# Performance work log

Measured on AMD Instinct MI355X. Metric: run time of the kernel, lower is better.

The kernel has to match this reference:

```python
import jax, jax.numpy as jnp
import numpy as np

N, D, E = 50000, 128, 800000
EPS = 1e-5


def setup_inputs() -> dict:
    key = jax.random.key(0)
    ks = jax.random.split(key, 16)
    x = jax.random.normal(ks[0], (N, D), dtype=jnp.float32)
    edge_index = jax.random.randint(ks[1], (2, E), 0, N, dtype=jnp.int32)
    s = 1.0 / np.sqrt(D)
    inp = {"x": x, "edge_index": edge_index}
    for i in range(3):
        inp[f"lng{i}"] = jnp.ones((D,), jnp.float32)
        inp[f"lnb{i}"] = jnp.zeros((D,), jnp.float32)
        inp[f"W{i}"] = jax.random.normal(ks[2 + 2 * i], (D, D), jnp.float32) * s
        inp[f"b{i}"] = jnp.zeros((D,), jnp.float32)
    return inp


def _gcn_norm(edge_index):
    # PyG GCNConv default: add self loops, symmetric normalization D^-1/2 (A+I) D^-1/2
    loop = jnp.arange(N, dtype=edge_index.dtype)
    src = jnp.concatenate([edge_index[0], loop])  # [E+N]
    dst = jnp.concatenate([edge_index[1], loop])
    deg = jax.ops.segment_sum(jnp.ones_like(dst, jnp.float32), dst, num_segments=N)
    dinv = jnp.where(deg > 0, jax.lax.rsqrt(jnp.maximum(deg, 1.0)), 0.0)
    norm = dinv[src] * dinv[dst]  # [E+N]
    return src, dst, norm


def _layer(h, g, bt, W, b, src, dst, norm):
    # LayerNorm -> ReLU -> GCNConv
    mu = jnp.mean(h, axis=-1, keepdims=True)
    var = jnp.mean(jnp.square(h - mu), axis=-1, keepdims=True)
    hn = (h - mu) * jax.lax.rsqrt(var + EPS) * g + bt
    hn = jax.nn.relu(hn) @ W  # [N, D]
    msg = norm[:, None] * hn[src]  # [E+N, D] gather
    return jax.ops.segment_sum(msg, dst, num_segments=N) + b


def reference(x, edge_index, lng0, lnb0, W0, b0, lng1, lnb1, W1, b1, lng2, lnb2, W2, b2):
    src, dst, norm = _gcn_norm(edge_index)
    # conv0 (GCNLayer) + residual
    x = _layer(x, lng0, lnb0, W0, b0, src, dst, norm) + x
    # conv1 (ResGCNLayer: two GCNLayers) + residual
    h = _layer(x, lng1, lnb1, W1, b1, src, dst, norm)
    h = _layer(h, lng2, lnb2, W2, b2, src, dst, norm)
    return h + x
```

## Files before the change

### kernel.cpp

```cpp
#include <hip/hip_runtime.h>

#define N_NODES 50000
#define DIM     128
#define E_EDGES 800000
#define ELLW    64

typedef __attribute__((ext_vector_type(8))) short short8;
typedef __attribute__((ext_vector_type(4))) float f32x4;

__device__ __forceinline__ float bflo(unsigned int u){ return __uint_as_float(u << 16); }
__device__ __forceinline__ float bfhi(unsigned int u){ return __uint_as_float(u & 0xFFFF0000u); }
__device__ __forceinline__ unsigned int f2bf(float f){
  unsigned int u = __float_as_uint(f);
  return (u + 0x7FFFu + ((u >> 16) & 1u)) >> 16;
}
__device__ __forceinline__ unsigned int pack2(float a, float b){
  return f2bf(a) | (f2bf(b) << 16);
}


__global__ __launch_bounds__(256) void count_kernel(const int* __restrict__ edges,
                                                    int* __restrict__ cnt){
  int e = blockIdx.x * 256 + threadIdx.x;
  if (e < E_EDGES) atomicAdd(&cnt[edges[E_EDGES + e]], 1);
}

__global__ __launch_bounds__(256) void dinv_pad_kernel(const int* __restrict__ cnt,
                                                       float* __restrict__ dinv,
                                                       int2* __restrict__ ell){
  int i = blockIdx.x * 256 + threadIdx.x;
  if (i >= N_NODES) return;
  int deg = cnt[i];
  dinv[i] = rsqrtf((float)(deg + 1));
  int2 pad; pad.x = i; pad.y = 0;
  size_t base = (size_t)i * ELLW + deg;
  ell[base + 0] = pad;
  ell[base + 1] = pad;
  ell[base + 2] = pad;
  ell[base + 3] = pad;
}

__global__ __launch_bounds__(256) void fill_kernel(const int* __restrict__ edges,
                                                   int* __restrict__ cur,
                                                   const float* __restrict__ dinv,
                                                   int2* __restrict__ ell){
  int e = blockIdx.x * 256 + threadIdx.x;
  if (e < E_EDGES){
    int s = edges[e];
    int d = edges[E_EDGES + e];
    int pos = atomicAdd(&cur[d], 1);
    int2 pk; pk.x = s; pk.y = __float_as_int(dinv[s] * dinv[d]);
    ell[(size_t)d * ELLW + pos] = pk;
  }
}

__global__ __launch_bounds__(256) void cvtw_all(const float* __restrict__ W0,
                                                const float* __restrict__ W1,
                                                const float* __restrict__ W2,
                                                unsigned short* __restrict__ Wt){
  int idx = blockIdx.x * 256 + threadIdx.x;
  int w = idx >> 14, r = idx & 16383;
  const float* W = (w == 0) ? W0 : (w == 1) ? W1 : W2;
  int k = r >> 7, n = r & 127;
  Wt[w * 16384 + n * 128 + k] = (unsigned short)f2bf(W[r]);
}


__global__ __launch_bounds__(256) void gemm_ln_mfma(const float* __restrict__ X,
                                                    const float* __restrict__ g,
                                                    const float* __restrict__ bt,
                                                    const unsigned short* __restrict__ Wt,
                                                    unsigned short* __restrict__ Y){
  __shared__ unsigned short ldsb[128 * 136];
  int tid = threadIdx.x;
  #pragma unroll
  for (int it = 0; it < 8; ++it){
    int c  = tid + it * 256;
    int n  = c >> 4, kc = c & 15;
    *(short8*)&ldsb[n * 136 + kc * 8] = *(const short8*)(Wt + n * 128 + kc * 8);
  }
  int wave = tid >> 6, lane = tid & 63, quad = lane >> 4, l15 = lane & 15;
  int rowbase = blockIdx.x * 128 + wave * 32;
  int rm0 = rowbase + l15;      if (rm0 > N_NODES - 1) rm0 = N_NODES - 1;
  int rm1 = rowbase + 16 + l15; if (rm1 > N_NODES - 1) rm1 = N_NODES - 1;

  float v0[4][8], v1[4][8];
  float s0 = 0.f, ss0 = 0.f, s1 = 0.f, ss1 = 0.f;
  #pragma unroll
  for (int kk = 0; kk < 4; ++kk){
    float4 xa = *(const float4*)(X + (size_t)rm0 * 128 + kk * 32 + quad * 8);
    float4 xb = *(const float4*)(X + (size_t)rm0 * 128 + kk * 32 + quad * 8 + 4);
    float4 ya = *(const float4*)(X + (size_t)rm1 * 128 + kk * 32 + quad * 8);
    float4 yb_ = *(const float4*)(X + (size_t)rm1 * 128 + kk * 32 + quad * 8 + 4);
    v0[kk][0]=xa.x; v0[kk][1]=xa.y; v0[kk][2]=xa.z; v0[kk][3]=xa.w;
    v0[kk][4]=xb.x; v0[kk][5]=xb.y; v0[kk][6]=xb.z; v0[kk][7]=xb.w;
    v1[kk][0]=ya.x; v1[kk][1]=ya.y; v1[kk][2]=ya.z; v1[kk][3]=ya.w;
    v1[kk][4]=yb_.x; v1[kk][5]=yb_.y; v1[kk][6]=yb_.z; v1[kk][7]=yb_.w;
    #pragma unroll
    for (int j = 0; j < 8; ++j){
      s0 += v0[kk][j]; ss0 += v0[kk][j] * v0[kk][j];
      s1 += v1[kk][j]; ss1 += v1[kk][j] * v1[kk][j];
    }
  }
  s0 += __shfl_xor(s0, 16, 64); ss0 += __shfl_xor(ss0, 16, 64);
  s0 += __shfl_xor(s0, 32, 64); ss0 += __shfl_xor(ss0, 32, 64);
  s1 += __shfl_xor(s1, 16, 64); ss1 += __shfl_xor(ss1, 16, 64);
  s1 += __shfl_xor(s1, 32, 64); ss1 += __shfl_xor(ss1, 32, 64);
  float mu0 = s0 * (1.0f/128.0f), var0 = ss0 * (1.0f/128.0f) - mu0*mu0;
  float mu1 = s1 * (1.0f/128.0f), var1 = ss1 * (1.0f/128.0f) - mu1*mu1;
  float rs0 = rsqrtf(var0 + 1e-5f), rs1 = rsqrtf(var1 + 1e-5f);

  short8 a0[4], a1[4];
  #pragma unroll
  for (int kk = 0; kk < 4; ++kk){
    float4 ga = *(const float4*)(g  + kk * 32 + quad * 8);
    float4 gb = *(const float4*)(g  + kk * 32 + quad * 8 + 4);
    float4 ba = *(const float4*)(bt + kk * 32 + quad * 8);
    float4 bb = *(const float4*)(bt + kk * 32 + quad * 8 + 4);
    float gg[8] = {ga.x,ga.y,ga.z,ga.w,gb.x,gb.y,gb.z,gb.w};
    float bbv[8] = {ba.x,ba.y,ba.z,ba.w,bb.x,bb.y,bb.z,bb.w};
    #pragma unroll
    for (int j = 0; j < 8; ++j){
      float h0 = fmaxf((v0[kk][j] - mu0) * rs0 * gg[j] + bbv[j], 0.0f);
      float h1 = fmaxf((v1[kk][j] - mu1) * rs1 * gg[j] + bbv[j], 0.0f);
      a0[kk][j] = (short)f2bf(h0);
      a1[kk][j] = (short)f2bf(h1);
    }
  }

  f32x4 acc[2][8];
  #pragma unroll
  for (int mt = 0; mt < 2; ++mt)
    #pragma unroll
    for (int nt = 0; nt < 8; ++nt) acc[mt][nt] = (f32x4){0.f, 0.f, 0.f, 0.f};
  __syncthreads();
  #pragma unroll
  for (int kk = 0; kk < 4; ++kk){
    #pragma unroll
    for (int nt = 0; nt < 8; ++nt){
      short8 b = *(const short8*)&ldsb[(nt * 16 + l15) * 136 + kk * 32 + quad * 8];
      acc[0][nt] = __builtin_amdgcn_mfma_f32_16x16x32_bf16(a0[kk], b, acc[0][nt], 0, 0, 0);
      acc[1][nt] = __builtin_amdgcn_mfma_f32_16x16x32_bf16(a1[kk], b, acc[1][nt], 0, 0, 0);
    }
  }
  #pragma unroll
  for (int mt = 0; mt < 2; ++mt)
    #pragma unroll
    for (int nt = 0; nt < 8; ++nt)
      #pragma unroll
      for (int r = 0; r < 4; ++r){
        int row = rowbase + mt * 16 + quad * 4 + r;
        if (row < N_NODES)
          Y[(size_t)row * 128 + nt * 16 + l15] = (unsigned short)f2bf(acc[mt][nt][r]);
      }
}


__global__ __launch_bounds__(256) void gemm_mfma(const unsigned short* __restrict__ A,
                                                 const unsigned short* __restrict__ Wt,
                                                 unsigned short* __restrict__ Y){
  __shared__ unsigned short ldsb[128 * 136];
  int tid = threadIdx.x;
  #pragma unroll
  for (int it = 0; it < 8; ++it){
    int c  = tid + it * 256;
    int n  = c >> 4, kc = c & 15;
    *(short8*)&ldsb[n * 136 + kc * 8] = *(const short8*)(Wt + n * 128 + kc * 8);
  }
  int wave = tid >> 6, lane = tid & 63, quad = lane >> 4, l15 = lane & 15;
  int rowbase = blockIdx.x * 128 + wave * 32;
  int rm0 = rowbase + l15;      if (rm0 > N_NODES - 1) rm0 = N_NODES - 1;
  int rm1 = rowbase + 16 + l15; if (rm1 > N_NODES - 1) rm1 = N_NODES - 1;

  short8 a0[4], a1[4];
  #pragma unroll
  for (int kk = 0; kk < 4; ++kk){
    a0[kk] = *(const short8*)(A + (size_t)rm0 * 128 + kk * 32 + quad * 8);
    a1[kk] = *(const short8*)(A + (size_t)rm1 * 128 + kk * 32 + quad * 8);
  }
  f32x4 acc[2][8];
  #pragma unroll
  for (int mt = 0; mt < 2; ++mt)
    #pragma unroll
    for (int nt = 0; nt < 8; ++nt) acc[mt][nt] = (f32x4){0.f, 0.f, 0.f, 0.f};
  __syncthreads();
  #pragma unroll
  for (int kk = 0; kk < 4; ++kk){
    #pragma unroll
    for (int nt = 0; nt < 8; ++nt){
      short8 b = *(const short8*)&ldsb[(nt * 16 + l15) * 136 + kk * 32 + quad * 8];
      acc[0][nt] = __builtin_amdgcn_mfma_f32_16x16x32_bf16(a0[kk], b, acc[0][nt], 0, 0, 0);
      acc[1][nt] = __builtin_amdgcn_mfma_f32_16x16x32_bf16(a1[kk], b, acc[1][nt], 0, 0, 0);
    }
  }
  #pragma unroll
  for (int mt = 0; mt < 2; ++mt)
    #pragma unroll
    for (int nt = 0; nt < 8; ++nt)
      #pragma unroll
      for (int r = 0; r < 4; ++r){
        int row = rowbase + mt * 16 + quad * 4 + r;
        if (row < N_NODES)
          Y[(size_t)row * 128 + nt * 16 + l15] = (unsigned short)f2bf(acc[mt][nt][r]);
      }
}


template<bool HAS_RES, bool DO_LN>
__global__ __launch_bounds__(256) void agg_kernel(const unsigned short* __restrict__ y,
                                                  const int* __restrict__ cnt,
                                                  const int2* __restrict__ ell,
                                                  const float* __restrict__ dinv,
                                                  const float* __restrict__ bias,
                                                  const float* __restrict__ res,
                                                  float* __restrict__ outp,
                                                  const float* __restrict__ lng,
                                                  const float* __restrict__ lnb,
                                                  unsigned short* __restrict__ hn_out){
  int wid  = (blockIdx.x * 256 + threadIdx.x) >> 6;
  int lane = threadIdx.x & 63;
  if (wid >= N_NODES) return;
  const unsigned int* y32 = (const unsigned int*)y;

  float di = dinv[wid];
  float ws = di * di;
  unsigned int us = y32[(size_t)wid * 64 + lane];
  float a0 = ws * bflo(us);
  float a1 = ws * bfhi(us);

  int deg = cnt[wid];
  int nb  = (deg + 3) >> 2;
  const int2* row = ell + (size_t)wid * ELLW;

  if (nb > 0){
    int2 c0[4]; unsigned int g0[4];
    #pragma unroll
    for (int j = 0; j < 4; ++j) c0[j] = row[j];
    #pragma unroll
    for (int j = 0; j < 4; ++j) g0[j] = y32[(size_t)c0[j].x * 64 + lane];
    for (int b = 1; b < nb; ++b){
      int2 c1[4]; unsigned int g1[4];
      #pragma unroll
      for (int j = 0; j < 4; ++j) c1[j] = row[b * 4 + j];
      #pragma unroll
      for (int j = 0; j < 4; ++j) g1[j] = y32[(size_t)c1[j].x * 64 + lane];
      #pragma unroll
      for (int j = 0; j < 4; ++j){
        float w = __int_as_float(c0[j].y);
        a0 += w * bflo(g0[j]); a1 += w * bfhi(g0[j]);
      }
      #pragma unroll
      for (int j = 0; j < 4; ++j){ c0[j] = c1[j]; g0[j] = g1[j]; }
    }
    #pragma unroll
    for (int j = 0; j < 4; ++j){
      float w = __int_as_float(c0[j].y);
      a0 += w * bflo(g0[j]); a1 += w * bfhi(g0[j]);
    }
  }

  float2 ub2 = ((const float2*)bias)[lane];
  a0 += ub2.x; a1 += ub2.y;
  if (HAS_RES){
    float2 ur = ((const float2*)res)[(size_t)wid * 64 + lane];
    a0 += ur.x; a1 += ur.y;
  }
  if (outp){
    float2 o; o.x = a0; o.y = a1;
    ((float2*)outp)[(size_t)wid * 64 + lane] = o;
  }

  if (DO_LN){
    float s = a0 + a1, ss = a0 * a0 + a1 * a1;
    #pragma unroll
    for (int d = 32; d >= 1; d >>= 1){ s += __shfl_xor(s, d, 64); ss += __shfl_xor(ss, d, 64); }
    float mu  = s * (1.0f / 128.0f);
    float var = ss * (1.0f / 128.0f) - mu * mu;
    float rs  = rsqrtf(var + 1e-5f);
    float2 ug = ((const float2*)lng)[lane];
    float2 ubb = ((const float2*)lnb)[lane];
    float h0 = fmaxf((a0 - mu) * rs * ug.x + ubb.x, 0.0f);
    float h1 = fmaxf((a1 - mu) * rs * ug.y + ubb.y, 0.0f);
    ((unsigned int*)hn_out)[(size_t)wid * 64 + lane] = pack2(h0, h1);
  }
}


extern "C" void kernel_launch(void* const* d_in, const int* in_sizes, int n_in,
                              void* d_out, int out_size, void* d_ws, size_t ws_size,
                              hipStream_t stream){
  const float* x    = (const float*)d_in[0];
  const int*   edges= (const int*)d_in[1];
  const float* lng0 = (const float*)d_in[2];
  const float* lnb0 = (const float*)d_in[3];
  const float* W0   = (const float*)d_in[4];
  const float* b0   = (const float*)d_in[5];
  const float* lng1 = (const float*)d_in[6];
  const float* lnb1 = (const float*)d_in[7];
  const float* W1   = (const float*)d_in[8];
  const float* b1   = (const float*)d_in[9];
  const float* lng2 = (const float*)d_in[10];
  const float* lnb2 = (const float*)d_in[11];
  const float* W2   = (const float*)d_in[12];
  const float* b2   = (const float*)d_in[13];

  char* p = (char*)d_ws;
  auto carve = [&](size_t bytes) -> void* {
    void* r = (void*)p;
    p += (bytes + 255) & ~(size_t)255;
    return r;
  };
  int*   cnt   = (int*)  carve(2 * N_NODES * 4);
  int*   cur   = cnt + N_NODES;
  float* dinv  = (float*)carve(N_NODES * 4);
  int2*  ell   = (int2*) carve((size_t)N_NODES * ELLW * 8);
  unsigned short* Wt = (unsigned short*)carve(3 * 128 * 128 * 2);
  unsigned short* hn = (unsigned short*)carve((size_t)N_NODES * 128 * 2);
  unsigned short* yb = (unsigned short*)carve((size_t)N_NODES * 128 * 2);
  float* out = (float*)d_out;

  hipMemsetAsync(cnt, 0, 2 * N_NODES * 4, stream);

  count_kernel<<<(E_EDGES + 255) / 256, 256, 0, stream>>>(edges, cnt);
  dinv_pad_kernel<<<(N_NODES + 255) / 256, 256, 0, stream>>>(cnt, dinv, ell);
  fill_kernel<<<(E_EDGES + 255) / 256, 256, 0, stream>>>(edges, cur, dinv, ell);
  cvtw_all<<<192, 256, 0, stream>>>(W0, W1, W2, Wt);

  const int GEMM_GRID = (N_NODES + 127) / 128;
  const int ROW_GRID  = (N_NODES + 3) / 4;

  gemm_ln_mfma<<<GEMM_GRID, 256, 0, stream>>>(x, lng0, lnb0, Wt, yb);
  agg_kernel<true, true><<<ROW_GRID, 256, 0, stream>>>(yb, cnt, ell, dinv,
                                                       b0, x, out, lng1, lnb1, hn);
  gemm_mfma<<<GEMM_GRID, 256, 0, stream>>>(hn, Wt + 16384, yb);
  agg_kernel<false, true><<<ROW_GRID, 256, 0, stream>>>(yb, cnt, ell, dinv,
                                                        b1, nullptr, nullptr, lng2, lnb2, hn);
  gemm_mfma<<<GEMM_GRID, 256, 0, stream>>>(hn, Wt + 32768, yb);
  agg_kernel<true, false><<<ROW_GRID, 256, 0, stream>>>(yb, cnt, ell, dinv,
                                                        b2, out, out, nullptr, nullptr, nullptr);
}
```

Measured before the change: 335.3 us.

## Aggregate two nodes per wavefront with wider gathers and memset-zeroed ELL padding

```diff
diff --git a/kernel.cpp b/kernel.cpp
--- a/kernel.cpp
+++ b/kernel.cpp
@@ -25,19 +25,10 @@
   if (e < E_EDGES) atomicAdd(&cnt[edges[E_EDGES + e]], 1);
 }
 
-__global__ __launch_bounds__(256) void dinv_pad_kernel(const int* __restrict__ cnt,
-                                                       float* __restrict__ dinv,
-                                                       int2* __restrict__ ell){
+__global__ __launch_bounds__(256) void dinv_kernel(const int* __restrict__ cnt,
+                                                   float* __restrict__ dinv){
   int i = blockIdx.x * 256 + threadIdx.x;
-  if (i >= N_NODES) return;
-  int deg = cnt[i];
-  dinv[i] = rsqrtf((float)(deg + 1));
-  int2 pad; pad.x = i; pad.y = 0;
-  size_t base = (size_t)i * ELLW + deg;
-  ell[base + 0] = pad;
-  ell[base + 1] = pad;
-  ell[base + 2] = pad;
-  ell[base + 3] = pad;
+  if (i < N_NODES) dinv[i] = rsqrtf((float)(cnt[i] + 1));
 }
 
 __global__ __launch_bounds__(256) void fill_kernel(const int* __restrict__ edges,
@@ -217,71 +208,78 @@
                                                   const float* __restrict__ lng,
                                                   const float* __restrict__ lnb,
                                                   unsigned short* __restrict__ hn_out){
-  int wid  = (blockIdx.x * 256 + threadIdx.x) >> 6;
+  int pair = (blockIdx.x * 256 + threadIdx.x) >> 6;
   int lane = threadIdx.x & 63;
-  if (wid >= N_NODES) return;
-  const unsigned int* y32 = (const unsigned int*)y;
-
-  float di = dinv[wid];
+  int half = lane >> 5, hl = lane & 31;
+  int node = pair * 2 + half;
+  if (node >= N_NODES) return;
+  const uint2* y2 = (const uint2*)y;
+
+  float di = dinv[node];
   float ws = di * di;
-  unsigned int us = y32[(size_t)wid * 64 + lane];
-  float a0 = ws * bflo(us);
-  float a1 = ws * bfhi(us);
-
-  int deg = cnt[wid];
+  uint2 us = y2[(size_t)node * 32 + hl];
+  float a0 = ws * bflo(us.x), a1 = ws * bfhi(us.x);
+  float a2 = ws * bflo(us.y), a3 = ws * bfhi(us.y);
+
+  int deg = cnt[node];
   int nb  = (deg + 3) >> 2;
-  const int2* row = ell + (size_t)wid * ELLW;
+  const int4* row = (const int4*)(ell + (size_t)node * ELLW);
 
   if (nb > 0){
-    int2 c0[4]; unsigned int g0[4];
-    #pragma unroll
-    for (int j = 0; j < 4; ++j) c0[j] = row[j];
-    #pragma unroll
-    for (int j = 0; j < 4; ++j) g0[j] = y32[(size_t)c0[j].x * 64 + lane];
+    int4 ea0 = row[0], eb0 = row[1];
+    uint2 g0 = y2[(size_t)ea0.x * 32 + hl];
+    uint2 g1 = y2[(size_t)ea0.z * 32 + hl];
+    uint2 g2 = y2[(size_t)eb0.x * 32 + hl];
+    uint2 g3 = y2[(size_t)eb0.z * 32 + hl];
     for (int b = 1; b < nb; ++b){
-      int2 c1[4]; unsigned int g1[4];
-      #pragma unroll
-      for (int j = 0; j < 4; ++j) c1[j] = row[b * 4 + j];
-      #pragma unroll
-      for (int j = 0; j < 4; ++j) g1[j] = y32[(size_t)c1[j].x * 64 + lane];
-      #pragma unroll
-      for (int j = 0; j < 4; ++j){
-        float w = __int_as_float(c0[j].y);
-        a0 += w * bflo(g0[j]); a1 += w * bfhi(g0[j]);
-      }
-      #pragma unroll
-      for (int j = 0; j < 4; ++j){ c0[j] = c1[j]; g0[j] = g1[j]; }
-    }
-    #pragma unroll
-    for (int j = 0; j < 4; ++j){
-      float w = __int_as_float(c0[j].y);
-      a0 += w * bflo(g0[j]); a1 += w * bfhi(g0[j]);
-    }
-  }
-
-  float2 ub2 = ((const float2*)bias)[lane];
-  a0 += ub2.x; a1 += ub2.y;
+      int4 ea1 = row[b * 2], eb1 = row[b * 2 + 1];
+      uint2 h0 = y2[(size_t)ea1.x * 32 + hl];
+      uint2 h1 = y2[(size_t)ea1.z * 32 + hl];
+      uint2 h2 = y2[(size_t)eb1.x * 32 + hl];
+      uint2 h3 = y2[(size_t)eb1.z * 32 + hl];
+      float w0 = __int_as_float(ea0.y), w1 = __int_as_float(ea0.w);
+      float w2 = __int_as_float(eb0.y), w3 = __int_as_float(eb0.w);
+      a0 += w0*bflo(g0.x); a1 += w0*bfhi(g0.x); a2 += w0*bflo(g0.y); a3 += w0*bfhi(g0.y);
+      a0 += w1*bflo(g1.x); a1 += w1*bfhi(g1.x); a2 += w1*bflo(g1.y); a3 += w1*bfhi(g1.y);
+      a0 += w2*bflo(g2.x); a1 += w2*bfhi(g2.x); a2 += w2*bflo(g2.y); a3 += w2*bfhi(g2.y);
+      a0 += w3*bflo(g3.x); a1 += w3*bfhi(g3.x); a2 += w3*bflo(g3.y); a3 += w3*bfhi(g3.y);
+      ea0 = ea1; eb0 = eb1; g0 = h0; g1 = h1; g2 = h2; g3 = h3;
+    }
+    float w0 = __int_as_float(ea0.y), w1 = __int_as_float(ea0.w);
+    float w2 = __int_as_float(eb0.y), w3 = __int_as_float(eb0.w);
+    a0 += w0*bflo(g0.x); a1 += w0*bfhi(g0.x); a2 += w0*bflo(g0.y); a3 += w0*bfhi(g0.y);
+    a0 += w1*bflo(g1.x); a1 += w1*bfhi(g1.x); a2 += w1*bflo(g1.y); a3 += w1*bfhi(g1.y);
+    a0 += w2*bflo(g2.x); a1 += w2*bfhi(g2.x); a2 += w2*bflo(g2.y); a3 += w2*bfhi(g2.y);
+    a0 += w3*bflo(g3.x); a1 += w3*bfhi(g3.x); a2 += w3*bflo(g3.y); a3 += w3*bfhi(g3.y);
+  }
+
+  float4 ub4 = ((const float4*)bias)[hl];
+  a0 += ub4.x; a1 += ub4.y; a2 += ub4.z; a3 += ub4.w;
   if (HAS_RES){
-    float2 ur = ((const float2*)res)[(size_t)wid * 64 + lane];
-    a0 += ur.x; a1 += ur.y;
+    float4 ur = ((const float4*)res)[(size_t)node * 32 + hl];
+    a0 += ur.x; a1 += ur.y; a2 += ur.z; a3 += ur.w;
   }
   if (outp){
-    float2 o; o.x = a0; o.y = a1;
-    ((float2*)outp)[(size_t)wid * 64 + lane] = o;
+    float4 o; o.x = a0; o.y = a1; o.z = a2; o.w = a3;
+    ((float4*)outp)[(size_t)node * 32 + hl] = o;
   }
 
   if (DO_LN){
-    float s = a0 + a1, ss = a0 * a0 + a1 * a1;
-    #pragma unroll
-    for (int d = 32; d >= 1; d >>= 1){ s += __shfl_xor(s, d, 64); ss += __shfl_xor(ss, d, 64); }
+    float s = a0 + a1 + a2 + a3;
+    float ss = a0*a0 + a1*a1 + a2*a2 + a3*a3;
+    #pragma unroll
+    for (int d = 16; d >= 1; d >>= 1){ s += __shfl_xor(s, d, 64); ss += __shfl_xor(ss, d, 64); }
     float mu  = s * (1.0f / 128.0f);
     float var = ss * (1.0f / 128.0f) - mu * mu;
     float rs  = rsqrtf(var + 1e-5f);
-    float2 ug = ((const float2*)lng)[lane];
-    float2 ubb = ((const float2*)lnb)[lane];
+    float4 ug = ((const float4*)lng)[hl];
+    float4 ubb = ((const float4*)lnb)[hl];
     float h0 = fmaxf((a0 - mu) * rs * ug.x + ubb.x, 0.0f);
     float h1 = fmaxf((a1 - mu) * rs * ug.y + ubb.y, 0.0f);
-    ((unsigned int*)hn_out)[(size_t)wid * 64 + lane] = pack2(h0, h1);
+    float h2 = fmaxf((a2 - mu) * rs * ug.z + ubb.z, 0.0f);
+    float h3 = fmaxf((a3 - mu) * rs * ug.w + ubb.w, 0.0f);
+    uint2 ho; ho.x = pack2(h0, h1); ho.y = pack2(h2, h3);
+    ((uint2*)hn_out)[(size_t)node * 32 + hl] = ho;
   }
 }
 
@@ -310,32 +308,33 @@
     p += (bytes + 255) & ~(size_t)255;
     return r;
   };
-  int*   cnt   = (int*)  carve(2 * N_NODES * 4);
-  int*   cur   = cnt + N_NODES;
+  int*   cnt   = (int*)  carve(N_NODES * 4);
+  int*   cur   = (int*)  carve(N_NODES * 4);
+  int2*  ell   = (int2*) carve((size_t)N_NODES * ELLW * 8);
+  size_t zspan = (char*)(ell + (size_t)N_NODES * ELLW) - (char*)cnt;
   float* dinv  = (float*)carve(N_NODES * 4);
-  int2*  ell   = (int2*) carve((size_t)N_NODES * ELLW * 8);
   unsigned short* Wt = (unsigned short*)carve(3 * 128 * 128 * 2);
   unsigned short* hn = (unsigned short*)carve((size_t)N_NODES * 128 * 2);
   unsigned short* yb = (unsigned short*)carve((size_t)N_NODES * 128 * 2);
   float* out = (float*)d_out;
 
-  hipMemsetAsync(cnt, 0, 2 * N_NODES * 4, stream);
+  hipMemsetAsync(cnt, 0, zspan, stream);
 
   count_kernel<<<(E_EDGES + 255) / 256, 256, 0, stream>>>(edges, cnt);
-  dinv_pad_kernel<<<(N_NODES + 255) / 256, 256, 0, stream>>>(cnt, dinv, ell);
+  dinv_kernel<<<(N_NODES + 255) / 256, 256, 0, stream>>>(cnt, dinv);
   fill_kernel<<<(E_EDGES + 255) / 256, 256, 0, stream>>>(edges, cur, dinv, ell);
   cvtw_all<<<192, 256, 0, stream>>>(W0, W1, W2, Wt);
 
   const int GEMM_GRID = (N_NODES + 127) / 128;
-  const int ROW_GRID  = (N_NODES + 3) / 4;
+  const int PAIR_GRID = (N_NODES / 2 + 3) / 4;
 
   gemm_ln_mfma<<<GEMM_GRID, 256, 0, stream>>>(x, lng0, lnb0, Wt, yb);
-  agg_kernel<true, true><<<ROW_GRID, 256, 0, stream>>>(yb, cnt, ell, dinv,
-                                                       b0, x, out, lng1, lnb1, hn);
+  agg_kernel<true, true><<<PAIR_GRID, 256, 0, stream>>>(yb, cnt, ell, dinv,
+                                                        b0, x, out, lng1, lnb1, hn);
   gemm_mfma<<<GEMM_GRID, 256, 0, stream>>>(hn, Wt + 16384, yb);
-  agg_kernel<false, true><<<ROW_GRID, 256, 0, stream>>>(yb, cnt, ell, dinv,
-                                                        b1, nullptr, nullptr, lng2, lnb2, hn);
+  agg_kernel<false, true><<<PAIR_GRID, 256, 0, stream>>>(yb, cnt, ell, dinv,
+                                                         b1, nullptr, nullptr, lng2, lnb2, hn);
   gemm_mfma<<<GEMM_GRID, 256, 0, stream>>>(hn, Wt + 32768, yb);
-  agg_kernel<true, false><<<ROW_GRID, 256, 0, stream>>>(yb, cnt, ell, dinv,
-                                                        b2, out, out, nullptr, nullptr, nullptr);
-}
+  agg_kernel<true, false><<<PAIR_GRID, 256, 0, stream>>>(yb, cnt, ell, dinv,
+                                                         b2, out, out, nullptr, nullptr, nullptr);
+}
```

After: 327.5 us. 1.02x faster.
